# Optimization experiments

Hardware: AMD Instinct MI355X
Metric: run time of the kernel (lower is better)

The kernel has to match this reference:

```python
import jax, jax.numpy as jnp
import numpy as np

E = 800_000
D = 64
N_NODES = 50_000


def setup_inputs() -> dict:
    key = jax.random.key(0)
    k1, k2, k3 = jax.random.split(key, 3)
    M = jax.random.normal(k1, (E, D), dtype=jnp.float32)
    edge_index = jax.random.randint(k2, (2, E), 0, N_NODES, dtype=jnp.int64)
    rev_index = jax.random.randint(k3, (E,), 0, E, dtype=jnp.int64)
    return {"M": M, "edge_index": edge_index, "rev_index": rev_index, "dim_size": N_NODES}


def reference(M, edge_index, rev_index, dim_size):
    # directed=True sum-aggregation variant of Aggregation.forward
    src, dest = edge_index[0], edge_index[1]
    # gather: scatter-add edge messages into destination nodes -> [dim_size, D]
    M_v = jax.ops.segment_sum(M, dest, num_segments=dim_size)
    # edge-wise gather by src node, minus reverse-edge message
    return M_v[src] - M[rev_index]
```

## Files before the change

kernel.cpp:

```cpp
#include <hip/hip_runtime.h>


#define D 64
#define N_NODES 50000
#define SCAN_THREADS 1024

typedef float f4 __attribute__((ext_vector_type(4)));

__global__ void agg_hist(const int* __restrict__ dest, int* __restrict__ counts, int E) {
    int t = blockIdx.x * blockDim.x + threadIdx.x;
    int e = t << 2;
    if (e + 3 < E) {
        int4 d = *reinterpret_cast<const int4*>(dest + e);
        atomicAdd(counts + d.x, 1);
        atomicAdd(counts + d.y, 1);
        atomicAdd(counts + d.z, 1);
        atomicAdd(counts + d.w, 1);
    } else {
        for (; e < E; ++e) atomicAdd(counts + dest[e], 1);
    }
}

__global__ void agg_scan(int* __restrict__ data, int* __restrict__ cursor) {
    __shared__ int wsums[SCAN_THREADS / 64];
    __shared__ int carry_sh;
    const int t = threadIdx.x;
    const int lane = t & 63;
    const int w = t >> 6;
    if (t == 0) carry_sh = 0;
    __syncthreads();
    for (int base = 0; base < N_NODES; base += SCAN_THREADS) {
        int i = base + t;
        int v = (i < N_NODES) ? data[i] : 0;
        int carry = carry_sh;
        int x = v;
        #pragma unroll
        for (int off = 1; off < 64; off <<= 1) {
            int y = __shfl_up(x, off, 64);
            if (lane >= off) x += y;
        }
        if (lane == 63) wsums[w] = x;
        __syncthreads();
        if (t == 0) {
            int run = 0;
            #pragma unroll
            for (int k = 0; k < SCAN_THREADS / 64; ++k) {
                int c = wsums[k]; wsums[k] = run; run += c;
            }
            carry_sh = carry + run;
        }
        __syncthreads();
        int excl = carry + wsums[w] + (x - v);
        if (i < N_NODES) { data[i] = excl; cursor[i] = excl; }
        __syncthreads();
    }
    if (t == 0) { data[N_NODES] = carry_sh; cursor[N_NODES] = carry_sh; }
}

__global__ void agg_bin(const int* __restrict__ dest, int* __restrict__ cursor,
                        int* __restrict__ order, int E) {
    int t = blockIdx.x * blockDim.x + threadIdx.x;
    int e = t << 2;
    if (e + 3 < E) {
        int4 d = *reinterpret_cast<const int4*>(dest + e);
        int p0 = atomicAdd(cursor + d.x, 1); order[p0] = e;
        int p1 = atomicAdd(cursor + d.y, 1); order[p1] = e + 1;
        int p2 = atomicAdd(cursor + d.z, 1); order[p2] = e + 2;
        int p3 = atomicAdd(cursor + d.w, 1); order[p3] = e + 3;
    } else {
        for (; e < E; ++e) {
            int pos = atomicAdd(cursor + dest[e], 1);
            order[pos] = e;
        }
    }
}

__global__ void agg_reduce(const float* __restrict__ M,
                           const int* __restrict__ order,
                           const int* __restrict__ offsets,
                           float* __restrict__ Mv) {
    int lane = threadIdx.x & 63;
    int node = (blockIdx.x * blockDim.x + threadIdx.x) >> 6;
    if (node >= N_NODES) return;
    int beg = offsets[node];
    int end = offsets[node + 1];
    float acc0 = 0.f, acc1 = 0.f, acc2 = 0.f, acc3 = 0.f;
    int i = beg;
    for (; i + 8 <= end; i += 8) {
        int e0 = order[i + 0], e1 = order[i + 1], e2 = order[i + 2], e3 = order[i + 3];
        int e4 = order[i + 4], e5 = order[i + 5], e6 = order[i + 6], e7 = order[i + 7];
        float a0 = M[(size_t)e0 * D + lane];
        float a1 = M[(size_t)e1 * D + lane];
        float a2 = M[(size_t)e2 * D + lane];
        float a3 = M[(size_t)e3 * D + lane];
        float a4 = M[(size_t)e4 * D + lane];
        float a5 = M[(size_t)e5 * D + lane];
        float a6 = M[(size_t)e6 * D + lane];
        float a7 = M[(size_t)e7 * D + lane];
        acc0 += a0 + a4;
        acc1 += a1 + a5;
        acc2 += a2 + a6;
        acc3 += a3 + a7;
    }
    for (; i < end; ++i) acc0 += M[(size_t)order[i] * D + lane];
    Mv[(size_t)node * D + lane] = (acc0 + acc1) + (acc2 + acc3);
}

__global__ void agg_gather(const float* __restrict__ Mv,
                           const float* __restrict__ M,
                           const int* __restrict__ src,
                           const int* __restrict__ rev,
                           float* __restrict__ out,
                           int E) {
    int gid = blockIdx.x * blockDim.x + threadIdx.x;
    int e  = gid >> 4;
    int c4 = gid & 15;
    if (e >= E) return;
    int s = src[e];
    int r = rev[e];
    f4 a = reinterpret_cast<const f4*>(Mv + (size_t)s * D)[c4];
    f4 b = reinterpret_cast<const f4*>(M  + (size_t)r * D)[c4];
    f4 o = a - b;
    __builtin_nontemporal_store(o, reinterpret_cast<f4*>(out + (size_t)e * D) + c4);
}

extern "C" void kernel_launch(void* const* d_in, const int* in_sizes, int n_in,
                              void* d_out, int out_size, void* d_ws, size_t ws_size,
                              hipStream_t stream) {
    const float* M   = (const float*)d_in[0];
    const int*   ei  = (const int*)d_in[1];
    const int*   rev = (const int*)d_in[2];

    int E = in_sizes[0] / D;
    const int* src  = ei;
    const int* dest = ei + E;

    int*   offsets = (int*)d_ws;
    int*   cursor  = offsets + 50304;
    int*   order   = cursor + 50304;
    float* Mv      = (float*)(order + 800128);

    hipMemsetAsync(offsets, 0, (N_NODES + 1) * sizeof(int), stream);

    int hb = ((E + 3) / 4 + 255) / 256;
    agg_hist<<<hb, 256, 0, stream>>>(dest, offsets, E);
    agg_scan<<<1, SCAN_THREADS, 0, stream>>>(offsets, cursor);
    agg_bin<<<hb, 256, 0, stream>>>(dest, cursor, order, E);

    int rb = (N_NODES * 64 + 255) / 256;
    agg_reduce<<<rb, 256, 0, stream>>>(M, order, offsets, Mv);

    int gb = (E * 16 + 255) / 256;
    agg_gather<<<gb, 256, 0, stream>>>(Mv, M, src, rev, (float*)d_out, E);
}
```

Measured before the change: 539.8 us.

## Scatter message rows into destination-sorted buffer and stream-reduce contiguously

```diff
diff --git a/kernel.cpp b/kernel.cpp
--- a/kernel.cpp
+++ b/kernel.cpp
@@ -6,6 +6,7 @@
 #define SCAN_THREADS 1024
 
 typedef float f4 __attribute__((ext_vector_type(4)));
+
 
 __global__ void agg_hist(const int* __restrict__ dest, int* __restrict__ counts, int E) {
     int t = blockIdx.x * blockDim.x + threadIdx.x;
@@ -57,6 +58,57 @@
     if (t == 0) { data[N_NODES] = carry_sh; cursor[N_NODES] = carry_sh; }
 }
 
+
+__global__ void agg_scatter(const float* __restrict__ M,
+                            const int* __restrict__ dest,
+                            int* __restrict__ cursor,
+                            float* __restrict__ Msort, int E) {
+    int gid = blockIdx.x * blockDim.x + threadIdx.x;
+    int e  = gid >> 4;
+    int c4 = gid & 15;
+    if (e >= E) return;
+    f4 v = reinterpret_cast<const f4*>(M + (size_t)e * D)[c4];
+    int pos = 0;
+    if (c4 == 0) pos = atomicAdd(cursor + dest[e], 1);
+    pos = __shfl(pos, (threadIdx.x & 63) & ~15, 64);
+    reinterpret_cast<f4*>(Msort + (size_t)pos * D)[c4] = v;
+}
+
+__global__ void agg_reduce_stream(const float* __restrict__ Msort,
+                                  const int* __restrict__ offsets,
+                                  float* __restrict__ Mv) {
+    int lane = threadIdx.x & 63;
+    int node = (blockIdx.x * blockDim.x + threadIdx.x) >> 6;
+    if (node >= N_NODES) return;
+    int beg = offsets[node];
+    int end = offsets[node + 1];
+    int c4 = lane & 15;
+    int rs = lane >> 4;
+    f4 acc0 = {0.f, 0.f, 0.f, 0.f}, acc1 = {0.f, 0.f, 0.f, 0.f};
+    int i = beg + rs;
+    for (; i + 4 < end; i += 8) {
+        f4 a = reinterpret_cast<const f4*>(Msort + (size_t)i * D)[c4];
+        f4 b = reinterpret_cast<const f4*>(Msort + (size_t)(i + 4) * D)[c4];
+        acc0 += a;
+        acc1 += b;
+    }
+    if (i < end)
+        acc0 += reinterpret_cast<const f4*>(Msort + (size_t)i * D)[c4];
+    acc0 += acc1;
+    #pragma unroll
+    for (int off = 16; off < 64; off <<= 1) {
+        f4 o;
+        o.x = __shfl_xor(acc0.x, off, 64);
+        o.y = __shfl_xor(acc0.y, off, 64);
+        o.z = __shfl_xor(acc0.z, off, 64);
+        o.w = __shfl_xor(acc0.w, off, 64);
+        acc0 += o;
+    }
+    if (rs == 0)
+        reinterpret_cast<f4*>(Mv + (size_t)node * D)[c4] = acc0;
+}
+
+
 __global__ void agg_bin(const int* __restrict__ dest, int* __restrict__ cursor,
                         int* __restrict__ order, int E) {
     int t = blockIdx.x * blockDim.x + threadIdx.x;
@@ -75,10 +127,10 @@
     }
 }
 
-__global__ void agg_reduce(const float* __restrict__ M,
-                           const int* __restrict__ order,
-                           const int* __restrict__ offsets,
-                           float* __restrict__ Mv) {
+__global__ void agg_reduce_order(const float* __restrict__ M,
+                                 const int* __restrict__ order,
+                                 const int* __restrict__ offsets,
+                                 float* __restrict__ Mv) {
     int lane = threadIdx.x & 63;
     int node = (blockIdx.x * blockDim.x + threadIdx.x) >> 6;
     if (node >= N_NODES) return;
@@ -106,6 +158,7 @@
     Mv[(size_t)node * D + lane] = (acc0 + acc1) + (acc2 + acc3);
 }
 
+
 __global__ void agg_gather(const float* __restrict__ Mv,
                            const float* __restrict__ M,
                            const int* __restrict__ src,
@@ -137,19 +190,31 @@
 
     int*   offsets = (int*)d_ws;
     int*   cursor  = offsets + 50304;
-    int*   order   = cursor + 50304;
-    float* Mv      = (float*)(order + 800128);
+    float* Mv      = (float*)(cursor + 50304);
+    float* Msort   = Mv + (size_t)N_NODES * D + 64;
+    int*   order   = (int*)Msort;
+
+    size_t need_scatter = ((size_t)(50304 + 50304) * 4)
+                        + ((size_t)N_NODES * D + 64) * 4
+                        + (size_t)E * D * 4;
+    bool scatter_path = ws_size >= need_scatter;
 
     hipMemsetAsync(offsets, 0, (N_NODES + 1) * sizeof(int), stream);
 
     int hb = ((E + 3) / 4 + 255) / 256;
     agg_hist<<<hb, 256, 0, stream>>>(dest, offsets, E);
     agg_scan<<<1, SCAN_THREADS, 0, stream>>>(offsets, cursor);
-    agg_bin<<<hb, 256, 0, stream>>>(dest, cursor, order, E);
 
     int rb = (N_NODES * 64 + 255) / 256;
-    agg_reduce<<<rb, 256, 0, stream>>>(M, order, offsets, Mv);
-
-    int gb = (E * 16 + 255) / 256;
+    if (scatter_path) {
+        int sb = ((size_t)E * 16 + 255) / 256;
+        agg_scatter<<<sb, 256, 0, stream>>>(M, dest, cursor, Msort, E);
+        agg_reduce_stream<<<rb, 256, 0, stream>>>(Msort, offsets, Mv);
+    } else {
+        agg_bin<<<hb, 256, 0, stream>>>(dest, cursor, order, E);
+        agg_reduce_order<<<rb, 256, 0, stream>>>(M, order, offsets, Mv);
+    }
+
+    int gb = ((size_t)E * 16 + 255) / 256;
     agg_gather<<<gb, 256, 0, stream>>>(Mv, M, src, rev, (float*)d_out, E);
 }
```

Measured after the change: 543.5 us. Within noise of the previous version (+0.7%).

## Replace single-block scan with atomic warp allocation; predicate reduce tail; gather two edges

Applied to the files above, without the earlier changes.

```diff
diff --git a/kernel.cpp b/kernel.cpp
--- a/kernel.cpp
+++ b/kernel.cpp
@@ -3,7 +3,6 @@
 
 #define D 64
 #define N_NODES 50000
-#define SCAN_THREADS 1024
 
 typedef float f4 __attribute__((ext_vector_type(4)));
 
@@ -21,40 +20,24 @@
     }
 }
 
-__global__ void agg_scan(int* __restrict__ data, int* __restrict__ cursor) {
-    __shared__ int wsums[SCAN_THREADS / 64];
-    __shared__ int carry_sh;
-    const int t = threadIdx.x;
-    const int lane = t & 63;
-    const int w = t >> 6;
-    if (t == 0) carry_sh = 0;
-    __syncthreads();
-    for (int base = 0; base < N_NODES; base += SCAN_THREADS) {
-        int i = base + t;
-        int v = (i < N_NODES) ? data[i] : 0;
-        int carry = carry_sh;
-        int x = v;
-        #pragma unroll
-        for (int off = 1; off < 64; off <<= 1) {
-            int y = __shfl_up(x, off, 64);
-            if (lane >= off) x += y;
-        }
-        if (lane == 63) wsums[w] = x;
-        __syncthreads();
-        if (t == 0) {
-            int run = 0;
-            #pragma unroll
-            for (int k = 0; k < SCAN_THREADS / 64; ++k) {
-                int c = wsums[k]; wsums[k] = run; run += c;
-            }
-            carry_sh = carry + run;
-        }
-        __syncthreads();
-        int excl = carry + wsums[w] + (x - v);
-        if (i < N_NODES) { data[i] = excl; cursor[i] = excl; }
-        __syncthreads();
+__global__ void agg_alloc(const int* __restrict__ counts,
+                          int* __restrict__ starts,
+                          int* __restrict__ cursor,
+                          int* __restrict__ gtotal, int N) {
+    int n = blockIdx.x * blockDim.x + threadIdx.x;
+    int lane = threadIdx.x & 63;
+    int c = (n < N) ? counts[n] : 0;
+    int x = c;
+    #pragma unroll
+    for (int off = 1; off < 64; off <<= 1) {
+        int y = __shfl_up(x, off, 64);
+        if (lane >= off) x += y;
     }
-    if (t == 0) { data[N_NODES] = carry_sh; cursor[N_NODES] = carry_sh; }
+    int base = 0;
+    if (lane == 63) base = atomicAdd(gtotal, x);
+    base = __shfl(base, 63, 64);
+    int s = base + x - c;
+    if (n < N) { starts[n] = s; cursor[n] = s; }
 }
 
 __global__ void agg_bin(const int* __restrict__ dest, int* __restrict__ cursor,
@@ -77,18 +60,26 @@
 
 __global__ void agg_reduce(const float* __restrict__ M,
                            const int* __restrict__ order,
-                           const int* __restrict__ offsets,
+                           const int* __restrict__ starts,
+                           const int* __restrict__ counts,
                            float* __restrict__ Mv) {
     int lane = threadIdx.x & 63;
     int node = (blockIdx.x * blockDim.x + threadIdx.x) >> 6;
     if (node >= N_NODES) return;
-    int beg = offsets[node];
-    int end = offsets[node + 1];
+    int beg = starts[node];
+    int end = beg + counts[node];
     float acc0 = 0.f, acc1 = 0.f, acc2 = 0.f, acc3 = 0.f;
-    int i = beg;
-    for (; i + 8 <= end; i += 8) {
-        int e0 = order[i + 0], e1 = order[i + 1], e2 = order[i + 2], e3 = order[i + 3];
-        int e4 = order[i + 4], e5 = order[i + 5], e6 = order[i + 6], e7 = order[i + 7];
+    for (int i = beg; i < end; i += 8) {
+        int j1 = (i + 1 < end) ? i + 1 : beg;
+        int j2 = (i + 2 < end) ? i + 2 : beg;
+        int j3 = (i + 3 < end) ? i + 3 : beg;
+        int j4 = (i + 4 < end) ? i + 4 : beg;
+        int j5 = (i + 5 < end) ? i + 5 : beg;
+        int j6 = (i + 6 < end) ? i + 6 : beg;
+        int j7 = (i + 7 < end) ? i + 7 : beg;
+        int e0 = order[i];
+        int e1 = order[j1], e2 = order[j2], e3 = order[j3];
+        int e4 = order[j4], e5 = order[j5], e6 = order[j6], e7 = order[j7];
         float a0 = M[(size_t)e0 * D + lane];
         float a1 = M[(size_t)e1 * D + lane];
         float a2 = M[(size_t)e2 * D + lane];
@@ -97,12 +88,18 @@
         float a5 = M[(size_t)e5 * D + lane];
         float a6 = M[(size_t)e6 * D + lane];
         float a7 = M[(size_t)e7 * D + lane];
+        a1 = (i + 1 < end) ? a1 : 0.f;
+        a2 = (i + 2 < end) ? a2 : 0.f;
+        a3 = (i + 3 < end) ? a3 : 0.f;
+        a4 = (i + 4 < end) ? a4 : 0.f;
+        a5 = (i + 5 < end) ? a5 : 0.f;
+        a6 = (i + 6 < end) ? a6 : 0.f;
+        a7 = (i + 7 < end) ? a7 : 0.f;
         acc0 += a0 + a4;
         acc1 += a1 + a5;
         acc2 += a2 + a6;
         acc3 += a3 + a7;
     }
-    for (; i < end; ++i) acc0 += M[(size_t)order[i] * D + lane];
     Mv[(size_t)node * D + lane] = (acc0 + acc1) + (acc2 + acc3);
 }
 
@@ -113,15 +110,24 @@
                            float* __restrict__ out,
                            int E) {
     int gid = blockIdx.x * blockDim.x + threadIdx.x;
-    int e  = gid >> 4;
+    int p  = gid >> 4;
     int c4 = gid & 15;
-    if (e >= E) return;
-    int s = src[e];
-    int r = rev[e];
-    f4 a = reinterpret_cast<const f4*>(Mv + (size_t)s * D)[c4];
-    f4 b = reinterpret_cast<const f4*>(M  + (size_t)r * D)[c4];
-    f4 o = a - b;
-    __builtin_nontemporal_store(o, reinterpret_cast<f4*>(out + (size_t)e * D) + c4);
+    int e0 = p << 1;
+    if (e0 >= E) return;
+    int e1 = e0 + 1;
+    int e1c = (e1 < E) ? e1 : e0;
+    int s0 = src[e0], r0 = rev[e0];
+    int s1 = src[e1c], r1 = rev[e1c];
+    f4 a0 = reinterpret_cast<const f4*>(Mv + (size_t)s0 * D)[c4];
+    f4 b0 = reinterpret_cast<const f4*>(M  + (size_t)r0 * D)[c4];
+    f4 a1 = reinterpret_cast<const f4*>(Mv + (size_t)s1 * D)[c4];
+    f4 b1 = reinterpret_cast<const f4*>(M  + (size_t)r1 * D)[c4];
+    f4 o0 = a0 - b0;
+    __builtin_nontemporal_store(o0, reinterpret_cast<f4*>(out + (size_t)e0 * D) + c4);
+    if (e1 < E) {
+        f4 o1 = a1 - b1;
+        __builtin_nontemporal_store(o1, reinterpret_cast<f4*>(out + (size_t)e1 * D) + c4);
+    }
 }
 
 extern "C" void kernel_launch(void* const* d_in, const int* in_sizes, int n_in,
@@ -135,21 +141,26 @@
     const int* src  = ei;
     const int* dest = ei + E;
 
-    int*   offsets = (int*)d_ws;
-    int*   cursor  = offsets + 50304;
-    int*   order   = cursor + 50304;
-    float* Mv      = (float*)(order + 800128);
+    int*   counts = (int*)d_ws;
+    int*   gtotal = counts + 50176;
+    int*   starts = gtotal + 64;
+    int*   cursor = starts + 50176;
+    int*   order  = cursor + 50176;
+    float* Mv     = (float*)(order + ((E + 63) & ~63));
 
-    hipMemsetAsync(offsets, 0, (N_NODES + 1) * sizeof(int), stream);
+    hipMemsetAsync(counts, 0, (50176 + 64) * sizeof(int), stream);
 
     int hb = ((E + 3) / 4 + 255) / 256;
-    agg_hist<<<hb, 256, 0, stream>>>(dest, offsets, E);
-    agg_scan<<<1, SCAN_THREADS, 0, stream>>>(offsets, cursor);
+    agg_hist<<<hb, 256, 0, stream>>>(dest, counts, E);
+
+    int ab = (N_NODES + 255) / 256;
+    agg_alloc<<<ab, 256, 0, stream>>>(counts, starts, cursor, gtotal, N_NODES);
+
     agg_bin<<<hb, 256, 0, stream>>>(dest, cursor, order, E);
 
     int rb = (N_NODES * 64 + 255) / 256;
-    agg_reduce<<<rb, 256, 0, stream>>>(M, order, offsets, Mv);
+    agg_reduce<<<rb, 256, 0, stream>>>(M, order, starts, counts, Mv);
 
-    int gb = (E * 16 + 255) / 256;
+    int gb = (int)(((size_t)(E / 2) * 16 + 255) / 256);
     agg_gather<<<gb, 256, 0, stream>>>(Mv, M, src, rev, (float*)d_out, E);
 }
```

New measurement: 496.7 us. -8.0%, faster.
